# Kernel tuning notes

Measured on AMD Instinct MI355X. Metric: run time of the kernel, lower is better.

Reference implementation:

```python
import jax, jax.numpy as jnp
import numpy as np
from jax import lax

F_DIM = 128
H_DIM = 128
K_NN = 16
S_PTS = 512
EPS = 1e-5


def _layernorm(x, g, b):
    m = jnp.mean(x, -1, keepdims=True)
    v = jnp.mean((x - m) ** 2, -1, keepdims=True)
    return (x - m) * lax.rsqrt(v + EPS) * g + b


def _batchnorm(x, g, b):
    # training-mode BN over (batch, points, neighbors) per channel; x: [B,S,K,C]
    m = jnp.mean(x, (0, 1, 2))
    v = jnp.mean((x - m) ** 2, (0, 1, 2))
    return (x - m) * lax.rsqrt(v + EPS) * g + b


def _gather(x, idx):
    # x: [B,R,C], idx: [B,...] int -> [B,...,C]
    return jax.vmap(lambda a, i: a[i])(x, idx)


def _fps(xyz, S):
    # farthest point sampling, deterministic start at index 0 (pytorch3d default)
    B, N, _ = xyz.shape
    idx0 = jnp.zeros((B,), jnp.int32)

    def step(carry, _):
        mind, last = carry
        p = jax.vmap(lambda a, i: a[i])(xyz, last)  # [B,3]
        d = jnp.sum((xyz - p[:, None]) ** 2, -1)  # [B,N]
        mind = jnp.minimum(mind, d)
        nxt = jnp.argmax(mind, -1).astype(jnp.int32)
        return (mind, nxt), nxt

    init = (jnp.full((B, N), 1e10, xyz.dtype), idx0)
    _, rest = lax.scan(step, init, None, length=S - 1)
    return jnp.concatenate([idx0[None], rest], 0).T  # [B,S]


def _knn_idx(q, ref, K):
    # squared dists [B,Q,R]; top-K nearest, sorted ascending by distance
    d2 = (jnp.sum(q * q, -1)[:, :, None] + jnp.sum(ref * ref, -1)[:, None, :]
          - 2.0 * jnp.einsum('bqd,brd->bqr', q, ref))
    _, idx = lax.top_k(-d2, K)
    return idx


def setup_inputs() -> dict:
    key = jax.random.key(0)
    ks = jax.random.split(key, 32)
    B, N, F, H = 4, 8192, F_DIM, H_DIM
    w = lambda k, shp: (jax.random.normal(k, shp, jnp.float32) * 0.02)
    return {
        'xyzp': jax.random.uniform(ks[0], (B, N, 4), jnp.float32),
        'features': jax.random.normal(ks[1], (B, N, F), jnp.float32),
        'ln_g': jnp.ones((F,), jnp.float32), 'ln_b': jnp.zeros((F,), jnp.float32),
        'td_w0': w(ks[2], (F + 3, F)), 'td_b0': jnp.zeros((F,), jnp.float32),
        'td_bn0_g': jnp.ones((F,), jnp.float32), 'td_bn0_b': jnp.zeros((F,), jnp.float32),
        'td_w1': w(ks[3], (F, F)), 'td_b1': jnp.zeros((F,), jnp.float32),
        'td_bn1_g': jnp.ones((F,), jnp.float32), 'td_bn1_b': jnp.zeros((F,), jnp.float32),
        'w_kern': w(ks[4], (F, H)), 'b_kern': jnp.zeros((H,), jnp.float32),
        'w_gkern': w(ks[5], (F, H)), 'b_gkern': jnp.zeros((H,), jnp.float32),
        'w_agg': w(ks[6], (H, F)), 'b_agg': jnp.zeros((F,), jnp.float32),
        'w_q': w(ks[7], (H, H)), 'w_k': w(ks[8], (H, H)), 'w_v': w(ks[9], (H, H)),
        'pe_w1': w(ks[10], (4, H)), 'pe_b1': jnp.zeros((H,), jnp.float32),
        'pe_w2': w(ks[11], (H, H)), 'pe_b2': jnp.zeros((H,), jnp.float32),
        'at_w1': w(ks[12], (H, H)), 'at_b1': jnp.zeros((H,), jnp.float32),
        'at_w2': w(ks[13], (H, H)), 'at_b2': jnp.zeros((H,), jnp.float32),
    }


def reference(xyzp, features, ln_g, ln_b, td_w0, td_b0, td_bn0_g, td_bn0_b,
              td_w1, td_b1, td_bn1_g, td_bn1_b, w_kern, b_kern, w_gkern, b_gkern,
              w_agg, b_agg, w_q, w_k, w_v, pe_w1, pe_b1, pe_w2, pe_b2,
              at_w1, at_b1, at_w2, at_b2):
    feats = _layernorm(features, ln_g, ln_b)
    xyz = xyzp[:, :, :3]
    # ---- TransitionDown ----
    fps_idx = _fps(xyz, S_PTS)                       # [B,S]
    new_xyz = _gather(xyz, fps_idx)                  # [B,S,3]
    idx_dn = _knn_idx(new_xyz, xyz, K_NN)            # [B,S,K]
    new_xyzp = _gather(xyzp, idx_dn)[:, :, 0]        # [B,S,4] nearest = self
    grouped_xyz = _gather(xyz, idx_dn) - new_xyz[:, :, None]   # [B,S,K,3]
    grouped_feat = _gather(feats, idx_dn)            # [B,S,K,F]
    h = jnp.concatenate([grouped_xyz, grouped_feat], -1)
    h = jax.nn.relu(_batchnorm(h @ td_w0 + td_b0, td_bn0_g, td_bn0_b))
    h = jax.nn.relu(_batchnorm(h @ td_w1 + td_b1, td_bn1_g, td_bn1_b))
    new_feats = jnp.max(h, axis=2)                   # [B,S,F]
    # ---- vector attention over K global neighbors ----
    idx_up = _knn_idx(xyz, new_xyz, K_NN)            # [B,N,K]
    pdiff = xyzp[:, :, None] - _gather(new_xyzp, idx_up)  # [B,N,K,4]
    pos_enc = jax.nn.relu(pdiff @ pe_w1 + pe_b1) @ pe_w2 + pe_b2
    x = feats @ w_kern + b_kern                      # [B,N,H]
    new_x = new_feats @ w_gkern + b_gkern            # [B,S,H]
    q = x @ w_q
    k = _gather(new_x @ w_k, idx_up)                 # [B,N,K,H]
    v = _gather(new_x @ w_v, idx_up)
    a = q[:, :, None] - k + pos_enc
    a = jax.nn.relu(a @ at_w1 + at_b1) @ at_w2 + at_b2
    a = jax.nn.softmax(a / np.float32(np.sqrt(H_DIM)), axis=2)  # softmax over neighbors
    res = jnp.sum(a * (v + pos_enc), axis=2)         # einsum bmnf,bmnf->bmf
    return res @ w_agg + b_agg + feats
```

## Files before the change

kernel.cpp:

```cpp
#include <hip/hip_runtime.h>

constexpr int B = 4, N = 8192, S = 512, K = 16, F = 128, H = 128;
constexpr float EPS = 1e-5f;

typedef short v8s __attribute__((ext_vector_type(8)));
typedef float v4f __attribute__((ext_vector_type(4)));

__device__ __forceinline__ short f2bf(float x) {
  union { float f; unsigned u; } v; v.f = x;
  unsigned r = v.u + 0x7fffu + ((v.u >> 16) & 1u);
  return (short)(r >> 16);
}
__device__ __forceinline__ float bf2f(short s) {
  union { unsigned u; float f; } v; v.u = ((unsigned)(unsigned short)s) << 16;
  return v.f;
}

template <int CTRL>
__device__ __forceinline__ float dpp_mov_f(float v) {
  return __int_as_float(__builtin_amdgcn_update_dpp(
      __float_as_int(v), __float_as_int(v), CTRL, 0xF, 0xF, false));
}
template <int CTRL>
__device__ __forceinline__ int dpp_mov_i(int v) {
  return __builtin_amdgcn_update_dpp(v, v, CTRL, 0xF, 0xF, false);
}

__global__ __launch_bounds__(256, 1) void front_kernel(
    const float* __restrict__ xyzp, float* __restrict__ new_xyz,
    const float* __restrict__ features, const float* __restrict__ ln_g,
    const float* __restrict__ ln_b, float* __restrict__ feats,
    const float* __restrict__ pe_w2, const float* __restrict__ at_w1,
    const float* __restrict__ at_w2, const float* __restrict__ w_kern,
    const float* __restrict__ w_q, const float* __restrict__ td_w1,
    const float* __restrict__ td_w0, short* __restrict__ wbf) {
  const int blk = blockIdx.x;
  const int t = threadIdx.x;
  if (blk >= 468) {
    int r = (blk - 468) * 4 + (t >> 6);
    int lane = t & 63;
    const float2* fp = (const float2*)(features + (size_t)r * F);
    float2 v = fp[lane];
    float s = v.x + v.y;
    #pragma unroll
    for (int off = 32; off > 0; off >>= 1) s += __shfl_xor(s, off);
    float m = s * (1.f / F);
    float dx = v.x - m, dy = v.y - m;
    float s2 = dx * dx + dy * dy;
    #pragma unroll
    for (int off = 32; off > 0; off >>= 1) s2 += __shfl_xor(s2, off);
    float rstd = rsqrtf(s2 * (1.f / F) + EPS);
    float2 gg = ((const float2*)ln_g)[lane];
    float2 bb = ((const float2*)ln_b)[lane];
    float2* op = (float2*)(feats + (size_t)r * F);
    op[lane] = make_float2(dx * rstd * gg.x + bb.x, dy * rstd * gg.y + bb.y);
    return;
  }
  if (blk >= 4) {
    int i = (blk - 4) * 256 + t;
    if (i < 6 * 16384) {
      int m = i >> 14, e = i & 16383;
      const float* src = m == 0 ? pe_w2 : m == 1 ? at_w1 : m == 2 ? at_w2
                       : m == 3 ? w_kern : m == 4 ? w_q : td_w1;
      int kx = e >> 7, n = e & 127;
      wbf[m * 16384 + n * 128 + kx] = f2bf(src[e]);
    } else {
      int e = i - 6 * 16384;
      int n = e / 160, kz = e % 160;
      short v = (kz < 131) ? f2bf(td_w0[kz * 128 + n]) : (short)0;
      wbf[6 * 16384 + n * 160 + kz] = v;
    }
    return;
  }
  __shared__ float4 xl4[N];
  __shared__ float nx[S * 3];
  __shared__ float2 slot[2][4];
  int b = blk;
  int lane = t & 63, wid = t >> 6;
  const float4* xp = (const float4*)(xyzp + (size_t)b * N * 4);
  float px[32], py[32], pz[32], mind[32];
  #pragma unroll
  for (int j = 0; j < 32; j++) {
    int idx = t + 256 * j;
    float4 p = xp[idx];
    px[j] = p.x; py[j] = p.y; pz[j] = p.z; mind[j] = 1e10f;
    xl4[idx] = p;
  }
  __syncthreads();
  float4 p0 = xl4[0];
  float cx = p0.x, cy = p0.y, cz = p0.z;
  if (t == 0) { nx[0] = cx; nx[1] = cy; nx[2] = cz; }
  for (int s = 1; s < S; ++s) {
    float bv = -1.f; int bj = 0;
    #pragma unroll
    for (int j = 0; j < 32; j++) {
      float dx = __fsub_rn(px[j], cx), dy = __fsub_rn(py[j], cy), dz = __fsub_rn(pz[j], cz);
      float d = __fadd_rn(__fadd_rn(__fmul_rn(dx, dx), __fmul_rn(dy, dy)), __fmul_rn(dz, dz));
      mind[j] = fminf(mind[j], d);
      if (mind[j] > bv) { bv = mind[j]; bj = j; }
    }
    int bi = t + (bj << 8);
    #define FPS_STEP(CTRL) { \
      float ov = dpp_mov_f<CTRL>(bv); int oi = dpp_mov_i<CTRL>(bi); \
      if (ov > bv || (ov == bv && oi < bi)) { bv = ov; bi = oi; } }
    FPS_STEP(0x111) FPS_STEP(0x112) FPS_STEP(0x114) FPS_STEP(0x118)
    FPS_STEP(0x142) FPS_STEP(0x143)
    #undef FPS_STEP
    int par = s & 1;
    if (lane == 63) slot[par][wid] = make_float2(bv, __int_as_float(bi));
    __syncthreads();
    float2 s0 = slot[par][0], s1 = slot[par][1], s2 = slot[par][2], s3 = slot[par][3];
    int i0 = __float_as_int(s0.y), i1 = __float_as_int(s1.y);
    int i2 = __float_as_int(s2.y), i3 = __float_as_int(s3.y);
    float4 c0v = xl4[i0], c1v = xl4[i1], c2v = xl4[i2], c3v = xl4[i3];
    float v0 = s0.x, v1 = s1.x, v2 = s2.x, v3 = s3.x;
    bool m01 = (v1 > v0) || (v1 == v0 && i1 < i0);
    float va = m01 ? v1 : v0; int ia = m01 ? i1 : i0;
    bool m23 = (v3 > v2) || (v3 == v2 && i3 < i2);
    float vb = m23 ? v3 : v2; int ib = m23 ? i3 : i2;
    bool mf = (vb > va) || (vb == va && ib < ia);
    float cax = m01 ? c1v.x : c0v.x, cay = m01 ? c1v.y : c0v.y, caz = m01 ? c1v.z : c0v.z;
    float cbx = m23 ? c3v.x : c2v.x, cby = m23 ? c3v.y : c2v.y, cbz = m23 ? c3v.z : c2v.z;
    cx = mf ? cbx : cax; cy = mf ? cby : cay; cz = mf ? cbz : caz;
    if (t == 0) { nx[s * 3 + 0] = cx; nx[s * 3 + 1] = cy; nx[s * 3 + 2] = cz; }
  }
  __syncthreads();
  for (int i = t; i < S * 3; i += 256)
    new_xyz[(size_t)b * S * 3 + i] = nx[i];
}

__global__ __launch_bounds__(256) void knn_dn_kernel(const float* __restrict__ xyzp,
    const float* __restrict__ new_xyz, int* __restrict__ idx_dn, float* __restrict__ new_xyzp) {
  int wave = threadIdx.x >> 6, lane = threadIdx.x & 63;
  int qid = blockIdx.x * 4 + wave;
  int b = qid >> 9, s = qid & (S - 1);
  const float4* xp = (const float4*)(xyzp + (size_t)b * N * 4);
  float qx = new_xyz[((size_t)b * S + s) * 3 + 0];
  float qy = new_xyz[((size_t)b * S + s) * 3 + 1];
  float qz = new_xyz[((size_t)b * S + s) * 3 + 2];
  float qq = __fadd_rn(__fadd_rn(__fmul_rn(qx, qx), __fmul_rn(qy, qy)), __fmul_rn(qz, qz));

  float lastD = -1.f; int lastI = -1;
  float D1, D2; int I1, I2;
  auto scan2 = [&]() {
    D1 = 3e38f; I1 = 0x7fffffff; D2 = 3e38f; I2 = 0x7fffffff;
    for (int j = 0; j < 128; j++) {
      int i = lane + 64 * j;
      float4 p = xp[i];
      float rr  = __fadd_rn(__fadd_rn(__fmul_rn(p.x, p.x), __fmul_rn(p.y, p.y)), __fmul_rn(p.z, p.z));
      float dot = __fadd_rn(__fadd_rn(__fmul_rn(qx, p.x), __fmul_rn(qy, p.y)), __fmul_rn(qz, p.z));
      float d2 = __fsub_rn(__fadd_rn(qq, rr), __fmul_rn(2.0f, dot));
      bool gate = (d2 > lastD) || (d2 == lastD && i > lastI);
      bool b1   = (d2 < D1) || (d2 == D1 && i < I1);
      bool b2   = (d2 < D2) || (d2 == D2 && i < I2);
      if (gate && b1)      { D2 = D1; I2 = I1; D1 = d2; I1 = i; }
      else if (gate && b2) { D2 = d2; I2 = i; }
    }
  };
  scan2();
  int outI = 0;
  float4 nn0;
  #pragma unroll 1
  for (int r = 0; r < K; r++) {
    float mD = D1; int mI = I1; int mL = lane;
    #pragma unroll
    for (int off = 32; off > 0; off >>= 1) {
      float od = __shfl_xor(mD, off); int oi = __shfl_xor(mI, off); int ol = __shfl_xor(mL, off);
      if (od < mD || (od == mD && oi < mI)) { mD = od; mI = oi; mL = ol; }
    }
    if (lane == r) outI = mI;
    if (r == 0 && lane == 0) nn0 = xp[mI];
    if (lane == mL) {
      lastD = mD; lastI = mI;
      if (I2 != 0x7fffffff) { D1 = D2; I1 = I2; D2 = 3e38f; I2 = 0x7fffffff; }
      else scan2();
    }
  }
  size_t base = ((size_t)b * S + s) * K;
  if (lane < K) idx_dn[base + lane] = outI;
  if (lane == 0) *(float4*)&new_xyzp[((size_t)b * S + s) * 4] = nn0;
}

__global__ __launch_bounds__(256) void knn_up_kernel(const float* __restrict__ xyzp,
    const float* __restrict__ new_xyz, int* __restrict__ idx_up) {
  int wave = threadIdx.x >> 6, lane = threadIdx.x & 63;
  int qid = blockIdx.x * 4 + wave;
  int b = qid >> 13, n = qid & (N - 1);
  const float4* xp = (const float4*)(xyzp + (size_t)b * N * 4);
  float4 qp = xp[n];
  float qx = qp.x, qy = qp.y, qz = qp.z;
  float qq = __fadd_rn(__fadd_rn(__fmul_rn(qx, qx), __fmul_rn(qy, qy)), __fmul_rn(qz, qz));
  float rx[8], ry[8], rz[8];
  #pragma unroll
  for (int j = 0; j < 8; j++) {
    int i = lane + 64 * j;
    rx[j] = new_xyz[((size_t)b * S + i) * 3 + 0];
    ry[j] = new_xyz[((size_t)b * S + i) * 3 + 1];
    rz[j] = new_xyz[((size_t)b * S + i) * 3 + 2];
  }
  float lastD = -1.f; int lastI = -1;
  float D1, D2; int I1, I2;
  auto scan2 = [&]() {
    D1 = 3e38f; I1 = 0x7fffffff; D2 = 3e38f; I2 = 0x7fffffff;
    #pragma unroll
    for (int j = 0; j < 8; j++) {
      int i = lane + 64 * j;
      float rr  = __fadd_rn(__fadd_rn(__fmul_rn(rx[j], rx[j]), __fmul_rn(ry[j], ry[j])), __fmul_rn(rz[j], rz[j]));
      float dot = __fadd_rn(__fadd_rn(__fmul_rn(qx, rx[j]), __fmul_rn(qy, ry[j])), __fmul_rn(qz, rz[j]));
      float d2 = __fsub_rn(__fadd_rn(qq, rr), __fmul_rn(2.0f, dot));
      bool gate = (d2 > lastD) || (d2 == lastD && i > lastI);
      bool b1   = (d2 < D1) || (d2 == D1 && i < I1);
      bool b2   = (d2 < D2) || (d2 == D2 && i < I2);
      if (gate && b1)      { D2 = D1; I2 = I1; D1 = d2; I1 = i; }
      else if (gate && b2) { D2 = d2; I2 = i; }
    }
  };
  scan2();
  int outI = 0;
  #pragma unroll 1
  for (int r = 0; r < K; r++) {
    float mD = D1; int mI = I1; int mL = lane;
    #pragma unroll
    for (int off = 32; off > 0; off >>= 1) {
      float od = __shfl_xor(mD, off); int oi = __shfl_xor(mI, off); int ol = __shfl_xor(mL, off);
      if (od < mD || (od == mD && oi < mI)) { mD = od; mI = oi; mL = ol; }
    }
    if (lane == r) outI = mI;
    if (lane == mL) {
      lastD = mD; lastI = mI;
      if (I2 != 0x7fffffff) { D1 = D2; I1 = I2; D2 = 3e38f; I2 = 0x7fffffff; }
      else scan2();
    }
  }
  size_t base = ((size_t)b * N + n) * K;
  if (lane < K) idx_up[base + lane] = outI;
}

constexpr int KS0 = 168;
__global__ __launch_bounds__(256) void td0_mfma(const float* __restrict__ xyzp,
    const float* __restrict__ new_xyz, const float* __restrict__ feats,
    const int* __restrict__ idx_dn, const short* __restrict__ w0bf, const float* __restrict__ b0,
    float* __restrict__ act0) {
  __shared__ short WT[128 * KS0];
  __shared__ short Abuf[4][16 * KS0];
  __shared__ int nbs[4][16];
  const int t = threadIdx.x, w = t >> 6, lane = t & 63;
  const int c0 = lane & 15, quad = lane >> 4;
  const int row0 = blockIdx.x * 64 + w * 16;
  const int bI = row0 >> 13;
  if (lane < 16) {
    int nb = idx_dn[row0 + lane];
    nbs[w][lane] = nb;
    int s = ((row0 + lane) >> 4) & (S - 1);
    #pragma unroll
    for (int d = 0; d < 3; d++)
      Abuf[w][lane * KS0 + d] =
          f2bf(xyzp[((size_t)bI * N + nb) * 4 + d] - new_xyz[((size_t)bI * S + s) * 3 + d]);
    for (int k2 = 131; k2 < 160; k2++) Abuf[w][lane * KS0 + k2] = 0;
  }
  #pragma unroll 4
  for (int i = 0; i < 32; i++) {
    int idx = lane + 64 * i;
    int r = idx >> 7, c = idx & 127;
    int nb = nbs[w][r];
    Abuf[w][r * KS0 + 3 + c] = f2bf(feats[((size_t)bI * N + nb) * F + c]);
  }
  #pragma unroll
  for (int i = 0; i < 10; i++) {
    int u = t + 256 * i;
    int n = u / 20, k8 = u % 20;
    *(v8s*)&WT[n * KS0 + k8 * 8] = *(const v8s*)&w0bf[n * 160 + k8 * 8];
  }
  __syncthreads();
  v4f acc[8];
  #pragma unroll
  for (int nt = 0; nt < 8; nt++) { float bvv = b0[nt * 16 + c0]; acc[nt] = (v4f){bvv, bvv, bvv, bvv}; }
  #pragma unroll
  for (int ks = 0; ks < 5; ks++) {
    v8s a = *(const v8s*)&Abuf[w][c0 * KS0 + ks * 32 + quad * 8];
    #pragma unroll
    for (int nt = 0; nt < 8; nt++) {
      v8s bf = *(const v8s*)&WT[(nt * 16 + c0) * KS0 + ks * 32 + quad * 8];
      acc[nt] = __builtin_amdgcn_mfma_f32_16x16x32_bf16(a, bf, acc[nt], 0, 0, 0);
    }
  }
  #pragma unroll
  for (int nt = 0; nt < 8; nt++)
    #pragma unroll
    for (int r = 0; r < 4; r++)
      act0[(size_t)(row0 + quad * 4 + r) * F + nt * 16 + c0] = acc[nt][r];
}

__global__ __launch_bounds__(256) void bn_reduce_kernel(const float* __restrict__ x,
                                                        float* __restrict__ sums) {
  __shared__ float ls[256], ls2[256];
  int t = threadIdx.x;
  size_t base = (size_t)blockIdx.x * 65536 + t;
  float s = 0.f, s2 = 0.f;
  for (int i = 0; i < 256; i++) {
    float v = x[base + (size_t)i * 256];
    s += v; s2 = fmaf(v, v, s2);
  }
  ls[t] = s; ls2[t] = s2; __syncthreads();
  if (t < 128) {
    s = ls[t] + ls[t + 128]; s2 = ls2[t] + ls2[t + 128];
    atomicAdd(&sums[t], s); atomicAdd(&sums[128 + t], s2);
  }
}

constexpr int KS1 = 136;
__global__ __launch_bounds__(256) void td1_mfma(const float* __restrict__ act0,
    const float* __restrict__ sums, const float* __restrict__ bn_g, const float* __restrict__ bn_b,
    const short* __restrict__ w1bf, const float* __restrict__ b1, float* __restrict__ act1) {
  __shared__ short WT[128 * KS1];
  __shared__ short Abuf[4][16 * KS1];
  __shared__ float scs[128], shs[128];
  const int t = threadIdx.x, w = t >> 6, lane = t & 63;
  const int c0 = lane & 15, quad = lane >> 4;
  const int row0 = blockIdx.x * 64 + w * 16;
  if (t < 128) {
    float m = sums[t] * (1.f / 32768.f);
    float var = sums[128 + t] * (1.f / 32768.f) - m * m;
    float rstd = rsqrtf(var + EPS);
    float sc = bn_g[t] * rstd;
    scs[t] = sc;
    shs[t] = bn_b[t] - m * sc;
  }
  #pragma unroll
  for (int i = 0; i < 8; i++) {
    int g = t + 256 * i;
    int n = g >> 4, k8 = g & 15;
    *(v8s*)&WT[n * KS1 + k8 * 8] = *(const v8s*)&w1bf[n * 128 + k8 * 8];
  }
  __syncthreads();
  #pragma unroll 4
  for (int i = 0; i < 32; i++) {
    int idx = lane + 64 * i;
    int r = idx >> 7, c = idx & 127;
    float vv = fmaxf(fmaf(act0[(size_t)(row0 + r) * F + c], scs[c], shs[c]), 0.f);
    Abuf[w][r * KS1 + c] = f2bf(vv);
  }
  v4f acc[8];
  #pragma unroll
  for (int nt = 0; nt < 8; nt++) { float bvv = b1[nt * 16 + c0]; acc[nt] = (v4f){bvv, bvv, bvv, bvv}; }
  #pragma unroll
  for (int ks = 0; ks < 4; ks++) {
    v8s a = *(const v8s*)&Abuf[w][c0 * KS1 + ks * 32 + quad * 8];
    #pragma unroll
    for (int nt = 0; nt < 8; nt++) {
      v8s bf = *(const v8s*)&WT[(nt * 16 + c0) * KS1 + ks * 32 + quad * 8];
      acc[nt] = __builtin_amdgcn_mfma_f32_16x16x32_bf16(a, bf, acc[nt], 0, 0, 0);
    }
  }
  #pragma unroll
  for (int nt = 0; nt < 8; nt++)
    #pragma unroll
    for (int r = 0; r < 4; r++)
      act1[(size_t)(row0 + quad * 4 + r) * F + nt * 16 + c0] = acc[nt][r];
}

__global__ __launch_bounds__(128) void tail_kernel(const float* __restrict__ act1,
    const float* __restrict__ sums, const float* __restrict__ bn_g, const float* __restrict__ bn_b,
    const float* __restrict__ w_gkern, const float* __restrict__ b_gkern,
    const float* __restrict__ wk, const float* __restrict__ wvp,
    float* __restrict__ kk, float* __restrict__ vv) {
  int bs = blockIdx.x, t = threadIdx.x;
  float m = sums[t] * (1.f / 32768.f);
  float var = sums[128 + t] * (1.f / 32768.f) - m * m;
  float rstd = rsqrtf(var + EPS);
  float sc = bn_g[t] * rstd;
  float sh = bn_b[t] - m * sc;
  float mx = -3e38f;
  for (int k = 0; k < K; k++) {
    float v = fmaxf(fmaf(act1[((size_t)bs * K + k) * F + t], sc, sh), 0.f);
    mx = fmaxf(mx, v);
  }
  __shared__ float row[128];
  __shared__ float row2[128];
  row[t] = mx; __syncthreads();
  {
    const float4* r4 = (const float4*)row;
    float a0 = 0.f, a1 = 0.f, a2 = 0.f, a3 = 0.f;
    #pragma unroll 8
    for (int i = 0; i < 32; i++) {
      float4 rv = r4[i];
      a0 = fmaf(rv.x, w_gkern[(4 * i + 0) * F + t], a0);
      a1 = fmaf(rv.y, w_gkern[(4 * i + 1) * F + t], a1);
      a2 = fmaf(rv.z, w_gkern[(4 * i + 2) * F + t], a2);
      a3 = fmaf(rv.w, w_gkern[(4 * i + 3) * F + t], a3);
    }
    row2[t] = b_gkern[t] + ((a0 + a1) + (a2 + a3));
  }
  __syncthreads();
  {
    const float4* r4 = (const float4*)row2;
    float k0 = 0.f, k1 = 0.f, k2 = 0.f, k3 = 0.f;
    float v0 = 0.f, v1 = 0.f, v2 = 0.f, v3 = 0.f;
    #pragma unroll 4
    for (int i = 0; i < 32; i++) {
      float4 rv = r4[i];
      k0 = fmaf(rv.x, wk[(4 * i + 0) * F + t], k0);
      k1 = fmaf(rv.y, wk[(4 * i + 1) * F + t], k1);
      k2 = fmaf(rv.z, wk[(4 * i + 2) * F + t], k2);
      k3 = fmaf(rv.w, wk[(4 * i + 3) * F + t], k3);
      v0 = fmaf(rv.x, wvp[(4 * i + 0) * F + t], v0);
      v1 = fmaf(rv.y, wvp[(4 * i + 1) * F + t], v1);
      v2 = fmaf(rv.z, wvp[(4 * i + 2) * F + t], v2);
      v3 = fmaf(rv.w, wvp[(4 * i + 3) * F + t], v3);
    }
    kk[(size_t)bs * F + t] = (k0 + k1) + (k2 + k3);
    vv[(size_t)bs * F + t] = (v0 + v1) + (v2 + v3);
  }
}

__global__ __launch_bounds__(256) void q_mfma(const float* __restrict__ feats,
    const short* __restrict__ wkbf, const float* __restrict__ b_kern,
    const short* __restrict__ wqbf, float* __restrict__ q) {
  __shared__ short WT[128 * KS1];
  __shared__ short Abuf[4][16 * KS1];
  const int t = threadIdx.x, w = t >> 6, lane = t & 63;
  const int c0 = lane & 15, quad = lane >> 4;
  const int row0 = blockIdx.x * 64 + w * 16;
  #pragma unroll 4
  for (int i = 0; i < 32; i++) {
    int idx = lane + 64 * i;
    int r = idx >> 7, c = idx & 127;
    Abuf[w][r * KS1 + c] = f2bf(feats[(size_t)(row0 + r) * F + c]);
  }
  #pragma unroll
  for (int i = 0; i < 8; i++) {
    int g = t + 256 * i;
    int n = g >> 4, k8 = g & 15;
    *(v8s*)&WT[n * KS1 + k8 * 8] = *(const v8s*)&wkbf[n * 128 + k8 * 8];
  }
  __syncthreads();
  v4f acc[8];
  #pragma unroll
  for (int nt = 0; nt < 8; nt++) { float bvv = b_kern[nt * 16 + c0]; acc[nt] = (v4f){bvv, bvv, bvv, bvv}; }
  #pragma unroll
  for (int ks = 0; ks < 4; ks++) {
    v8s a = *(const v8s*)&Abuf[w][c0 * KS1 + ks * 32 + quad * 8];
    #pragma unroll
    for (int nt = 0; nt < 8; nt++) {
      v8s bf = *(const v8s*)&WT[(nt * 16 + c0) * KS1 + ks * 32 + quad * 8];
      acc[nt] = __builtin_amdgcn_mfma_f32_16x16x32_bf16(a, bf, acc[nt], 0, 0, 0);
    }
  }
  __syncthreads();
  #pragma unroll
  for (int i = 0; i < 8; i++) {
    int g = t + 256 * i;
    int n = g >> 4, k8 = g & 15;
    *(v8s*)&WT[n * KS1 + k8 * 8] = *(const v8s*)&wqbf[n * 128 + k8 * 8];
  }
  #pragma unroll
  for (int nt = 0; nt < 8; nt++)
    #pragma unroll
    for (int r = 0; r < 4; r++)
      Abuf[w][(quad * 4 + r) * KS1 + nt * 16 + c0] = f2bf(acc[nt][r]);
  __syncthreads();
  v4f acc2[8];
  #pragma unroll
  for (int nt = 0; nt < 8; nt++) acc2[nt] = (v4f){0.f, 0.f, 0.f, 0.f};
  #pragma unroll
  for (int ks = 0; ks < 4; ks++) {
    v8s a = *(const v8s*)&Abuf[w][c0 * KS1 + ks * 32 + quad * 8];
    #pragma unroll
    for (int nt = 0; nt < 8; nt++) {
      v8s bf = *(const v8s*)&WT[(nt * 16 + c0) * KS1 + ks * 32 + quad * 8];
      acc2[nt] = __builtin_amdgcn_mfma_f32_16x16x32_bf16(a, bf, acc2[nt], 0, 0, 0);
    }
  }
  #pragma unroll
  for (int nt = 0; nt < 8; nt++)
    #pragma unroll
    for (int r = 0; r < 4; r++)
      q[(size_t)(row0 + quad * 4 + r) * F + nt * 16 + c0] = acc2[nt][r];
}

constexpr int WS = 136;
constexpr int VS = 132;

__global__ __launch_bounds__(256) void attn_kernel(const float* __restrict__ xyzp,
    const float* __restrict__ q, const float* __restrict__ kk, const float* __restrict__ vv,
    const float* __restrict__ new_xyzp, const int* __restrict__ idx_up,
    const float* __restrict__ feats, const short* __restrict__ wbf,
    const float* __restrict__ pe_w1, const float* __restrict__ pe_b1,
    const float* __restrict__ pe_b2,
    const float* __restrict__ at_b1, const float* __restrict__ at_b2,
    const float* __restrict__ w_agg, const float* __restrict__ b_agg,
    float* __restrict__ out) {
  __shared__ short WT[128 * WS];
  __shared__ short Abuf[4][16 * WS];
  __shared__ short WVb[4][16 * VS];
  __shared__ float qsh[4][128];
  __shared__ float resh[4][128];
  __shared__ float pdsh[4][16][4];
  __shared__ int   nbsh[4][16];

  const int t = threadIdx.x, w = t >> 6, lane = t & 63;
  const int c0 = lane & 15, quad = lane >> 4;
  const int p = blockIdx.x * 4 + w;
  const int b = p >> 13;

  qsh[w][lane]      = q[(size_t)p * H + lane];
  qsh[w][lane + 64] = q[(size_t)p * H + lane + 64];
  if (lane < 16) nbsh[w][lane] = idx_up[(size_t)p * K + lane];
  {
    int k = lane >> 2, d = lane & 3;
    pdsh[w][k][d] = xyzp[(size_t)p * 4 + d] - new_xyzp[((size_t)b * S + nbsh[w][k]) * 4 + d];
  }
  #pragma unroll
  for (int cc = 0; cc < 2; cc++) {
    int c = cc * 64 + lane;
    float bb = pe_b1[c];
    float w0 = pe_w1[c], w1 = pe_w1[128 + c], w2 = pe_w1[256 + c], w3 = pe_w1[384 + c];
    #pragma unroll
    for (int k = 0; k < 16; k++) {
      float h = bb + pdsh[w][k][0] * w0 + pdsh[w][k][1] * w1 + pdsh[w][k][2] * w2 + pdsh[w][k][3] * w3;
      Abuf[w][k * WS + c] = f2bf(fmaxf(h, 0.f));
    }
  }

  auto stageW = [&](const short* __restrict__ Wt) {
    __syncthreads();
    #pragma unroll
    for (int i = 0; i < 8; i++) {
      int g = t + 256 * i;
      int n = g >> 4, k8 = g & 15;
      *(v8s*)&WT[n * WS + k8 * 8] = *(const v8s*)&Wt[n * 128 + k8 * 8];
    }
    __syncthreads();
  };
  auto gemm = [&](const float* __restrict__ bias, v4f* acc) {
    #pragma unroll
    for (int nt = 0; nt < 8; nt++) {
      float bv = bias[nt * 16 + c0];
      acc[nt] = (v4f){bv, bv, bv, bv};
    }
    #pragma unroll
    for (int ks = 0; ks < 4; ks++) {
      v8s a = *(const v8s*)&Abuf[w][c0 * WS + ks * 32 + quad * 8];
      #pragma unroll
      for (int nt = 0; nt < 8; nt++) {
        v8s bf = *(const v8s*)&WT[(nt * 16 + c0) * WS + ks * 32 + quad * 8];
        acc[nt] = __builtin_amdgcn_mfma_f32_16x16x32_bf16(a, bf, acc[nt], 0, 0, 0);
      }
    }
  };

  stageW(wbf + 0 * 16384);
  v4f pe[8];
  gemm(pe_b2, pe);

  #pragma unroll
  for (int nt = 0; nt < 8; nt++) {
    #pragma unroll
    for (int r = 0; r < 4; r++) {
      int krow = quad * 4 + r;
      int c = nt * 16 + c0;
      int nb = nbsh[w][krow];
      float pev = pe[nt][r];
      float avv = qsh[w][c] - kk[((size_t)b * S + nb) * H + c] + pev;
      float wvv = vv[((size_t)b * S + nb) * H + c] + pev;
      Abuf[w][krow * WS + c] = f2bf(avv);
      WVb[w][krow * VS + c] = f2bf(wvv);
    }
  }

  stageW(wbf + 1 * 16384);
  v4f h1[8];
  gemm(at_b1, h1);
  #pragma unroll
  for (int nt = 0; nt < 8; nt++)
    #pragma unroll
    for (int r = 0; r < 4; r++)
      Abuf[w][(quad * 4 + r) * WS + nt * 16 + c0] = f2bf(fmaxf(h1[nt][r], 0.f));

  stageW(wbf + 2 * 16384);
  v4f lg[8];
  gemm(at_b2, lg);

  const float scale = 0.08838834764831845f;
  #pragma unroll
  for (int nt = 0; nt < 8; nt++) {
    float l0 = lg[nt][0] * scale, l1 = lg[nt][1] * scale;
    float l2 = lg[nt][2] * scale, l3 = lg[nt][3] * scale;
    float m = fmaxf(fmaxf(l0, l1), fmaxf(l2, l3));
    m = fmaxf(m, __shfl_xor(m, 16));
    m = fmaxf(m, __shfl_xor(m, 32));
    float e0 = expf(l0 - m), e1 = expf(l1 - m), e2 = expf(l2 - m), e3 = expf(l3 - m);
    float ssum = e0 + e1 + e2 + e3;
    ssum += __shfl_xor(ssum, 16);
    ssum += __shfl_xor(ssum, 32);
    float inv = 1.f / ssum;
    int c = nt * 16 + c0;
    float partial =
        e0 * bf2f(WVb[w][(quad * 4 + 0) * VS + c]) + e1 * bf2f(WVb[w][(quad * 4 + 1) * VS + c]) +
        e2 * bf2f(WVb[w][(quad * 4 + 2) * VS + c]) + e3 * bf2f(WVb[w][(quad * 4 + 3) * VS + c]);
    partial += __shfl_xor(partial, 16);
    partial += __shfl_xor(partial, 32);
    if (quad == 0) resh[w][c] = partial * inv;
  }
  __syncthreads();

  #pragma unroll
  for (int cc = 0; cc < 2; cc++) {
    int c = cc * 64 + lane;
    const float4* r4 = (const float4*)resh[w];
    float o0 = 0.f, o1 = 0.f, o2 = 0.f, o3 = 0.f;
    #pragma unroll 4
    for (int i = 0; i < 32; i++) {
      float4 rv = r4[i];
      o0 = fmaf(rv.x, w_agg[(4 * i + 0) * H + c], o0);
      o1 = fmaf(rv.y, w_agg[(4 * i + 1) * H + c], o1);
      o2 = fmaf(rv.z, w_agg[(4 * i + 2) * H + c], o2);
      o3 = fmaf(rv.w, w_agg[(4 * i + 3) * H + c], o3);
    }
    float o = b_agg[c] + ((o0 + o1) + (o2 + o3));
    out[(size_t)p * F + c] = o + feats[(size_t)p * F + c];
  }
}

extern "C" void kernel_launch(void* const* d_in, const int* in_sizes, int n_in,
                              void* d_out, int out_size, void* d_ws, size_t ws_size,
                              hipStream_t stream) {
  (void)in_sizes; (void)n_in; (void)out_size; (void)ws_size;
  const float* xyzp    = (const float*)d_in[0];
  const float* features= (const float*)d_in[1];
  const float* ln_g    = (const float*)d_in[2];
  const float* ln_b    = (const float*)d_in[3];
  const float* td_w0   = (const float*)d_in[4];
  const float* td_b0   = (const float*)d_in[5];
  const float* bn0_g   = (const float*)d_in[6];
  const float* bn0_b   = (const float*)d_in[7];
  const float* td_w1   = (const float*)d_in[8];
  const float* td_b1   = (const float*)d_in[9];
  const float* bn1_g   = (const float*)d_in[10];
  const float* bn1_b   = (const float*)d_in[11];
  const float* w_kern  = (const float*)d_in[12];
  const float* b_kern  = (const float*)d_in[13];
  const float* w_gkern = (const float*)d_in[14];
  const float* b_gkern = (const float*)d_in[15];
  const float* w_agg   = (const float*)d_in[16];
  const float* b_agg   = (const float*)d_in[17];
  const float* w_q     = (const float*)d_in[18];
  const float* w_k     = (const float*)d_in[19];
  const float* w_v     = (const float*)d_in[20];
  const float* pe_w1   = (const float*)d_in[21];
  const float* pe_b1   = (const float*)d_in[22];
  const float* pe_w2   = (const float*)d_in[23];
  const float* pe_b2   = (const float*)d_in[24];
  const float* at_w1   = (const float*)d_in[25];
  const float* at_b1   = (const float*)d_in[26];
  const float* at_w2   = (const float*)d_in[27];
  const float* at_b2   = (const float*)d_in[28];
  float* out = (float*)d_out;

  float* wsf = (float*)d_ws;
  float* feats     = wsf + 0;
  float* q         = wsf + 4194304;
  float* act0      = wsf + 8388608;
  float* act1      = wsf + 12582912;
  short* wbf       = (short*)(wsf + 16777216);
  float* kk        = wsf + 17301504;
  float* vv        = wsf + 17563648;
  float* new_xyz   = wsf + 17825792;
  float* new_xyzp  = wsf + 17831936;
  float* sums0     = wsf + 17840128;
  float* sums1     = wsf + 17840384;
  int* idx_dn  = (int*)(wsf + 17841152);
  int* idx_up  = idx_dn + 32768;

  hipMemsetAsync(sums0, 0, 512 * sizeof(float), stream);
  front_kernel<<<4 + 464 + B * N / 4, 256, 0, stream>>>(
      xyzp, new_xyz, features, ln_g, ln_b, feats,
      pe_w2, at_w1, at_w2, w_kern, w_q, td_w1, td_w0, wbf);
  knn_dn_kernel<<<512, 256, 0, stream>>>(xyzp, new_xyz, idx_dn, new_xyzp);
  knn_up_kernel<<<8192, 256, 0, stream>>>(xyzp, new_xyz, idx_up);
  td0_mfma<<<512, 256, 0, stream>>>(xyzp, new_xyz, feats, idx_dn, wbf + 6 * 16384, td_b0, act0);
  bn_reduce_kernel<<<64, 256, 0, stream>>>(act0, sums0);
  td1_mfma<<<512, 256, 0, stream>>>(act0, sums0, bn0_g, bn0_b, wbf + 5 * 16384, td_b1, act1);
  bn_reduce_kernel<<<64, 256, 0, stream>>>(act1, sums1);
  tail_kernel<<<B * S, 128, 0, stream>>>(act1, sums1, bn1_g, bn1_b,
      w_gkern, b_gkern, w_k, w_v, kk, vv);
  q_mfma<<<512, 256, 0, stream>>>(feats, wbf + 3 * 16384, b_kern, wbf + 4 * 16384, q);
  attn_kernel<<<8192, 256, 0, stream>>>(xyzp, q, kk, vv, new_xyzp, idx_up, feats, wbf,
      pe_w1, pe_b1, pe_b2, at_b1, at_b2, w_agg, b_agg, out);
}
```

Measured before the change: 1.593 ms.

## Overlap q projection with FPS and merge both KNN kernels into one launch

LayerNorm and the weight conversion move into a separate pre_kernel. The q projection GEMM blocks are folded into front_kernel so they run beside the four serial farthest-point-sampling blocks. knn_dn and knn_up are merged into a single mid_kernel launch. The aim is to fill idle CUs during the long FPS phase and cut launch and tail gaps. The cost is an extra launch, and the q blocks now use front_kernel's large LDS allocation with launch_bounds(256,1), which limits their occupancy.

```diff
diff --git a/kernel.cpp b/kernel.cpp
--- a/kernel.cpp
+++ b/kernel.cpp
@@ -2,6 +2,8 @@
 
 constexpr int B = 4, N = 8192, S = 512, K = 16, F = 128, H = 128;
 constexpr float EPS = 1e-5f;
+constexpr int KS0 = 168;
+constexpr int KS1 = 136;
 
 typedef short v8s __attribute__((ext_vector_type(8)));
 typedef float v4f __attribute__((ext_vector_type(4)));
@@ -26,18 +28,16 @@
   return __builtin_amdgcn_update_dpp(v, v, CTRL, 0xF, 0xF, false);
 }
 
-__global__ __launch_bounds__(256, 1) void front_kernel(
-    const float* __restrict__ xyzp, float* __restrict__ new_xyz,
+__global__ __launch_bounds__(256) void pre_kernel(
     const float* __restrict__ features, const float* __restrict__ ln_g,
     const float* __restrict__ ln_b, float* __restrict__ feats,
     const float* __restrict__ pe_w2, const float* __restrict__ at_w1,
     const float* __restrict__ at_w2, const float* __restrict__ w_kern,
     const float* __restrict__ w_q, const float* __restrict__ td_w1,
     const float* __restrict__ td_w0, short* __restrict__ wbf) {
-  const int blk = blockIdx.x;
-  const int t = threadIdx.x;
-  if (blk >= 468) {
-    int r = (blk - 468) * 4 + (t >> 6);
+  const int blk = blockIdx.x, t = threadIdx.x;
+  if (blk < 8192) {
+    int r = blk * 4 + (t >> 6);
     int lane = t & 63;
     const float2* fp = (const float2*)(features + (size_t)r * F);
     float2 v = fp[lane];
@@ -56,25 +56,95 @@
     op[lane] = make_float2(dx * rstd * gg.x + bb.x, dy * rstd * gg.y + bb.y);
     return;
   }
-  if (blk >= 4) {
-    int i = (blk - 4) * 256 + t;
-    if (i < 6 * 16384) {
-      int m = i >> 14, e = i & 16383;
-      const float* src = m == 0 ? pe_w2 : m == 1 ? at_w1 : m == 2 ? at_w2
-                       : m == 3 ? w_kern : m == 4 ? w_q : td_w1;
-      int kx = e >> 7, n = e & 127;
-      wbf[m * 16384 + n * 128 + kx] = f2bf(src[e]);
-    } else {
-      int e = i - 6 * 16384;
-      int n = e / 160, kz = e % 160;
-      short v = (kz < 131) ? f2bf(td_w0[kz * 128 + n]) : (short)0;
-      wbf[6 * 16384 + n * 160 + kz] = v;
-    }
-    return;
-  }
+  int i = (blk - 8192) * 256 + t;
+  if (i < 6 * 16384) {
+    int m = i >> 14, e = i & 16383;
+    const float* src = m == 0 ? pe_w2 : m == 1 ? at_w1 : m == 2 ? at_w2
+                     : m == 3 ? w_kern : m == 4 ? w_q : td_w1;
+    int kx = e >> 7, n = e & 127;
+    wbf[m * 16384 + n * 128 + kx] = f2bf(src[e]);
+  } else {
+    int e = i - 6 * 16384;
+    int n = e / 160, kz = e % 160;
+    short v = (kz < 131) ? f2bf(td_w0[kz * 128 + n]) : (short)0;
+    wbf[6 * 16384 + n * 160 + kz] = v;
+  }
+}
+
+__global__ __launch_bounds__(256, 1) void front_kernel(
+    const float* __restrict__ xyzp, float* __restrict__ new_xyz,
+    const float* __restrict__ feats, const short* __restrict__ wkbf,
+    const float* __restrict__ b_kern, const short* __restrict__ wqbf,
+    float* __restrict__ q) {
   __shared__ float4 xl4[N];
   __shared__ float nx[S * 3];
   __shared__ float2 slot[2][4];
+  const int blk = blockIdx.x;
+  const int t = threadIdx.x;
+  if (blk >= 4) {
+    short* WT  = (short*)xl4;
+    short* AbB = ((short*)xl4) + 128 * KS1;
+    const int w = t >> 6, lane = t & 63;
+    const int c0 = lane & 15, quad = lane >> 4;
+    const int row0 = (blk - 4) * 64 + w * 16;
+    short* Ab = AbB + w * 16 * KS1;
+    #pragma unroll 4
+    for (int i = 0; i < 32; i++) {
+      int idx = lane + 64 * i;
+      int r = idx >> 7, c = idx & 127;
+      Ab[r * KS1 + c] = f2bf(feats[(size_t)(row0 + r) * F + c]);
+    }
+    #pragma unroll
+    for (int i = 0; i < 8; i++) {
+      int g = t + 256 * i;
+      int n = g >> 4, k8 = g & 15;
+      *(v8s*)&WT[n * KS1 + k8 * 8] = *(const v8s*)&wkbf[n * 128 + k8 * 8];
+    }
+    __syncthreads();
+    v4f acc[8];
+    #pragma unroll
+    for (int nt = 0; nt < 8; nt++) { float bvv = b_kern[nt * 16 + c0]; acc[nt] = (v4f){bvv, bvv, bvv, bvv}; }
+    #pragma unroll
+    for (int ks = 0; ks < 4; ks++) {
+      v8s a = *(const v8s*)&Ab[c0 * KS1 + ks * 32 + quad * 8];
+      #pragma unroll
+      for (int nt = 0; nt < 8; nt++) {
+        v8s bf = *(const v8s*)&WT[(nt * 16 + c0) * KS1 + ks * 32 + quad * 8];
+        acc[nt] = __builtin_amdgcn_mfma_f32_16x16x32_bf16(a, bf, acc[nt], 0, 0, 0);
+      }
+    }
+    __syncthreads();
+    #pragma unroll
+    for (int i = 0; i < 8; i++) {
+      int g = t + 256 * i;
+      int n = g >> 4, k8 = g & 15;
+      *(v8s*)&WT[n * KS1 + k8 * 8] = *(const v8s*)&wqbf[n * 128 + k8 * 8];
+    }
+    #pragma unroll
+    for (int nt = 0; nt < 8; nt++)
+      #pragma unroll
+      for (int r = 0; r < 4; r++)
+        Ab[(quad * 4 + r) * KS1 + nt * 16 + c0] = f2bf(acc[nt][r]);
+    __syncthreads();
+    v4f acc2[8];
+    #pragma unroll
+    for (int nt = 0; nt < 8; nt++) acc2[nt] = (v4f){0.f, 0.f, 0.f, 0.f};
+    #pragma unroll
+    for (int ks = 0; ks < 4; ks++) {
+      v8s a = *(const v8s*)&Ab[c0 * KS1 + ks * 32 + quad * 8];
+      #pragma unroll
+      for (int nt = 0; nt < 8; nt++) {
+        v8s bf = *(const v8s*)&WT[(nt * 16 + c0) * KS1 + ks * 32 + quad * 8];
+        acc2[nt] = __builtin_amdgcn_mfma_f32_16x16x32_bf16(a, bf, acc2[nt], 0, 0, 0);
+      }
+    }
+    #pragma unroll
+    for (int nt = 0; nt < 8; nt++)
+      #pragma unroll
+      for (int r = 0; r < 4; r++)
+        q[(size_t)(row0 + quad * 4 + r) * F + nt * 16 + c0] = acc2[nt][r];
+    return;
+  }
   int b = blk;
   int lane = t & 63, wid = t >> 6;
   const float4* xp = (const float4*)(xyzp + (size_t)b * N * 4);
@@ -129,62 +199,61 @@
     new_xyz[(size_t)b * S * 3 + i] = nx[i];
 }
 
-__global__ __launch_bounds__(256) void knn_dn_kernel(const float* __restrict__ xyzp,
-    const float* __restrict__ new_xyz, int* __restrict__ idx_dn, float* __restrict__ new_xyzp) {
+__global__ __launch_bounds__(256) void mid_kernel(const float* __restrict__ xyzp,
+    const float* __restrict__ new_xyz, int* __restrict__ idx_dn,
+    float* __restrict__ new_xyzp, int* __restrict__ idx_up) {
+  const int blk = blockIdx.x;
   int wave = threadIdx.x >> 6, lane = threadIdx.x & 63;
-  int qid = blockIdx.x * 4 + wave;
-  int b = qid >> 9, s = qid & (S - 1);
-  const float4* xp = (const float4*)(xyzp + (size_t)b * N * 4);
-  float qx = new_xyz[((size_t)b * S + s) * 3 + 0];
-  float qy = new_xyz[((size_t)b * S + s) * 3 + 1];
-  float qz = new_xyz[((size_t)b * S + s) * 3 + 2];
-  float qq = __fadd_rn(__fadd_rn(__fmul_rn(qx, qx), __fmul_rn(qy, qy)), __fmul_rn(qz, qz));
-
-  float lastD = -1.f; int lastI = -1;
-  float D1, D2; int I1, I2;
-  auto scan2 = [&]() {
-    D1 = 3e38f; I1 = 0x7fffffff; D2 = 3e38f; I2 = 0x7fffffff;
-    for (int j = 0; j < 128; j++) {
-      int i = lane + 64 * j;
-      float4 p = xp[i];
-      float rr  = __fadd_rn(__fadd_rn(__fmul_rn(p.x, p.x), __fmul_rn(p.y, p.y)), __fmul_rn(p.z, p.z));
-      float dot = __fadd_rn(__fadd_rn(__fmul_rn(qx, p.x), __fmul_rn(qy, p.y)), __fmul_rn(qz, p.z));
-      float d2 = __fsub_rn(__fadd_rn(qq, rr), __fmul_rn(2.0f, dot));
-      bool gate = (d2 > lastD) || (d2 == lastD && i > lastI);
-      bool b1   = (d2 < D1) || (d2 == D1 && i < I1);
-      bool b2   = (d2 < D2) || (d2 == D2 && i < I2);
-      if (gate && b1)      { D2 = D1; I2 = I1; D1 = d2; I1 = i; }
-      else if (gate && b2) { D2 = d2; I2 = i; }
-    }
-  };
-  scan2();
-  int outI = 0;
-  float4 nn0;
-  #pragma unroll 1
-  for (int r = 0; r < K; r++) {
-    float mD = D1; int mI = I1; int mL = lane;
-    #pragma unroll
-    for (int off = 32; off > 0; off >>= 1) {
-      float od = __shfl_xor(mD, off); int oi = __shfl_xor(mI, off); int ol = __shfl_xor(mL, off);
-      if (od < mD || (od == mD && oi < mI)) { mD = od; mI = oi; mL = ol; }
-    }
-    if (lane == r) outI = mI;
-    if (r == 0 && lane == 0) nn0 = xp[mI];
-    if (lane == mL) {
-      lastD = mD; lastI = mI;
-      if (I2 != 0x7fffffff) { D1 = D2; I1 = I2; D2 = 3e38f; I2 = 0x7fffffff; }
-      else scan2();
-    }
-  }
-  size_t base = ((size_t)b * S + s) * K;
-  if (lane < K) idx_dn[base + lane] = outI;
-  if (lane == 0) *(float4*)&new_xyzp[((size_t)b * S + s) * 4] = nn0;
-}
-
-__global__ __launch_bounds__(256) void knn_up_kernel(const float* __restrict__ xyzp,
-    const float* __restrict__ new_xyz, int* __restrict__ idx_up) {
-  int wave = threadIdx.x >> 6, lane = threadIdx.x & 63;
-  int qid = blockIdx.x * 4 + wave;
+  if (blk < 512) {
+    int qid = blk * 4 + wave;
+    int b = qid >> 9, s = qid & (S - 1);
+    const float4* xp = (const float4*)(xyzp + (size_t)b * N * 4);
+    float qx = new_xyz[((size_t)b * S + s) * 3 + 0];
+    float qy = new_xyz[((size_t)b * S + s) * 3 + 1];
+    float qz = new_xyz[((size_t)b * S + s) * 3 + 2];
+    float qq = __fadd_rn(__fadd_rn(__fmul_rn(qx, qx), __fmul_rn(qy, qy)), __fmul_rn(qz, qz));
+    float lastD = -1.f; int lastI = -1;
+    float D1, D2; int I1, I2;
+    auto scan2 = [&]() {
+      D1 = 3e38f; I1 = 0x7fffffff; D2 = 3e38f; I2 = 0x7fffffff;
+      for (int j = 0; j < 128; j++) {
+        int i = lane + 64 * j;
+        float4 p = xp[i];
+        float rr  = __fadd_rn(__fadd_rn(__fmul_rn(p.x, p.x), __fmul_rn(p.y, p.y)), __fmul_rn(p.z, p.z));
+        float dot = __fadd_rn(__fadd_rn(__fmul_rn(qx, p.x), __fmul_rn(qy, p.y)), __fmul_rn(qz, p.z));
+        float d2 = __fsub_rn(__fadd_rn(qq, rr), __fmul_rn(2.0f, dot));
+        bool gate = (d2 > lastD) || (d2 == lastD && i > lastI);
+        bool b1   = (d2 < D1) || (d2 == D1 && i < I1);
+        bool b2   = (d2 < D2) || (d2 == D2 && i < I2);
+        if (gate && b1)      { D2 = D1; I2 = I1; D1 = d2; I1 = i; }
+        else if (gate && b2) { D2 = d2; I2 = i; }
+      }
+    };
+    scan2();
+    int outI = 0;
+    float4 nn0;
+    #pragma unroll 1
+    for (int r = 0; r < K; r++) {
+      float mD = D1; int mI = I1; int mL = lane;
+      #pragma unroll
+      for (int off = 32; off > 0; off >>= 1) {
+        float od = __shfl_xor(mD, off); int oi = __shfl_xor(mI, off); int ol = __shfl_xor(mL, off);
+        if (od < mD || (od == mD && oi < mI)) { mD = od; mI = oi; mL = ol; }
+      }
+      if (lane == r) outI = mI;
+      if (r == 0 && lane == 0) nn0 = xp[mI];
+      if (lane == mL) {
+        lastD = mD; lastI = mI;
+        if (I2 != 0x7fffffff) { D1 = D2; I1 = I2; D2 = 3e38f; I2 = 0x7fffffff; }
+        else scan2();
+      }
+    }
+    size_t base = ((size_t)b * S + s) * K;
+    if (lane < K) idx_dn[base + lane] = outI;
+    if (lane == 0) *(float4*)&new_xyzp[((size_t)b * S + s) * 4] = nn0;
+    return;
+  }
+  int qid = (blk - 512) * 4 + wave;
   int b = qid >> 13, n = qid & (N - 1);
   const float4* xp = (const float4*)(xyzp + (size_t)b * N * 4);
   float4 qp = xp[n];
@@ -236,7 +305,6 @@
   if (lane < K) idx_up[base + lane] = outI;
 }
 
-constexpr int KS0 = 168;
 __global__ __launch_bounds__(256) void td0_mfma(const float* __restrict__ xyzp,
     const float* __restrict__ new_xyz, const float* __restrict__ feats,
     const int* __restrict__ idx_dn, const short* __restrict__ w0bf, const float* __restrict__ b0,
@@ -308,7 +376,6 @@
   }
 }
 
-constexpr int KS1 = 136;
 __global__ __launch_bounds__(256) void td1_mfma(const float* __restrict__ act0,
     const float* __restrict__ sums, const float* __restrict__ bn_g, const float* __restrict__ bn_b,
     const short* __restrict__ w1bf, const float* __restrict__ b1, float* __restrict__ act1) {
@@ -411,71 +478,6 @@
     kk[(size_t)bs * F + t] = (k0 + k1) + (k2 + k3);
     vv[(size_t)bs * F + t] = (v0 + v1) + (v2 + v3);
   }
-}
-
-__global__ __launch_bounds__(256) void q_mfma(const float* __restrict__ feats,
-    const short* __restrict__ wkbf, const float* __restrict__ b_kern,
-    const short* __restrict__ wqbf, float* __restrict__ q) {
-  __shared__ short WT[128 * KS1];
-  __shared__ short Abuf[4][16 * KS1];
-  const int t = threadIdx.x, w = t >> 6, lane = t & 63;
-  const int c0 = lane & 15, quad = lane >> 4;
-  const int row0 = blockIdx.x * 64 + w * 16;
-  #pragma unroll 4
-  for (int i = 0; i < 32; i++) {
-    int idx = lane + 64 * i;
-    int r = idx >> 7, c = idx & 127;
-    Abuf[w][r * KS1 + c] = f2bf(feats[(size_t)(row0 + r) * F + c]);
-  }
-  #pragma unroll
-  for (int i = 0; i < 8; i++) {
-    int g = t + 256 * i;
-    int n = g >> 4, k8 = g & 15;
-    *(v8s*)&WT[n * KS1 + k8 * 8] = *(const v8s*)&wkbf[n * 128 + k8 * 8];
-  }
-  __syncthreads();
-  v4f acc[8];
-  #pragma unroll
-  for (int nt = 0; nt < 8; nt++) { float bvv = b_kern[nt * 16 + c0]; acc[nt] = (v4f){bvv, bvv, bvv, bvv}; }
-  #pragma unroll
-  for (int ks = 0; ks < 4; ks++) {
-    v8s a = *(const v8s*)&Abuf[w][c0 * KS1 + ks * 32 + quad * 8];
-    #pragma unroll
-    for (int nt = 0; nt < 8; nt++) {
-      v8s bf = *(const v8s*)&WT[(nt * 16 + c0) * KS1 + ks * 32 + quad * 8];
-      acc[nt] = __builtin_amdgcn_mfma_f32_16x16x32_bf16(a, bf, acc[nt], 0, 0, 0);
-    }
-  }
-  __syncthreads();
-  #pragma unroll
-  for (int i = 0; i < 8; i++) {
-    int g = t + 256 * i;
-    int n = g >> 4, k8 = g & 15;
-    *(v8s*)&WT[n * KS1 + k8 * 8] = *(const v8s*)&wqbf[n * 128 + k8 * 8];
-  }
-  #pragma unroll
-  for (int nt = 0; nt < 8; nt++)
-    #pragma unroll
-    for (int r = 0; r < 4; r++)
-      Abuf[w][(quad * 4 + r) * KS1 + nt * 16 + c0] = f2bf(acc[nt][r]);
-  __syncthreads();
-  v4f acc2[8];
-  #pragma unroll
-  for (int nt = 0; nt < 8; nt++) acc2[nt] = (v4f){0.f, 0.f, 0.f, 0.f};
-  #pragma unroll
-  for (int ks = 0; ks < 4; ks++) {
-    v8s a = *(const v8s*)&Abuf[w][c0 * KS1 + ks * 32 + quad * 8];
-    #pragma unroll
-    for (int nt = 0; nt < 8; nt++) {
-      v8s bf = *(const v8s*)&WT[(nt * 16 + c0) * KS1 + ks * 32 + quad * 8];
-      acc2[nt] = __builtin_amdgcn_mfma_f32_16x16x32_bf16(a, bf, acc2[nt], 0, 0, 0);
-    }
-  }
-  #pragma unroll
-  for (int nt = 0; nt < 8; nt++)
-    #pragma unroll
-    for (int r = 0; r < 4; r++)
-      q[(size_t)(row0 + quad * 4 + r) * F + nt * 16 + c0] = acc2[nt][r];
 }
 
 constexpr int WS = 136;
@@ -673,18 +675,17 @@
   int* idx_up  = idx_dn + 32768;
 
   hipMemsetAsync(sums0, 0, 512 * sizeof(float), stream);
-  front_kernel<<<4 + 464 + B * N / 4, 256, 0, stream>>>(
-      xyzp, new_xyz, features, ln_g, ln_b, feats,
+  pre_kernel<<<8192 + 464, 256, 0, stream>>>(features, ln_g, ln_b, feats,
       pe_w2, at_w1, at_w2, w_kern, w_q, td_w1, td_w0, wbf);
-  knn_dn_kernel<<<512, 256, 0, stream>>>(xyzp, new_xyz, idx_dn, new_xyzp);
-  knn_up_kernel<<<8192, 256, 0, stream>>>(xyzp, new_xyz, idx_up);
+  front_kernel<<<4 + 512, 256, 0, stream>>>(xyzp, new_xyz, feats,
+      wbf + 3 * 16384, b_kern, wbf + 4 * 16384, q);
+  mid_kernel<<<512 + 8192, 256, 0, stream>>>(xyzp, new_xyz, idx_dn, new_xyzp, idx_up);
   td0_mfma<<<512, 256, 0, stream>>>(xyzp, new_xyz, feats, idx_dn, wbf + 6 * 16384, td_b0, act0);
   bn_reduce_kernel<<<64, 256, 0, stream>>>(act0, sums0);
   td1_mfma<<<512, 256, 0, stream>>>(act0, sums0, bn0_g, bn0_b, wbf + 5 * 16384, td_b1, act1);
   bn_reduce_kernel<<<64, 256, 0, stream>>>(act1, sums1);
   tail_kernel<<<B * S, 128, 0, stream>>>(act1, sums1, bn1_g, bn1_b,
       w_gkern, b_gkern, w_k, w_v, kk, vv);
-  q_mfma<<<512, 256, 0, stream>>>(feats, wbf + 3 * 16384, b_kern, wbf + 4 * 16384, q);
   attn_kernel<<<8192, 256, 0, stream>>>(xyzp, q, kk, vv, new_xyzp, idx_up, feats, wbf,
       pe_w1, pe_b1, pe_b2, at_b1, at_b2, w_agg, b_agg, out);
 }
```

Result: faster. 1.483 ms (median of 2 runs) (-6.9%).
